# Optimization experiments

Hardware: AMD Instinct MI355X
Metric: run time of the kernel (lower is better)

## Reference

```python
import jax, jax.numpy as jnp
import numpy as np

N_NODES = 50000
N_EDGES = 800000
N_GRAPHS = 64


def graph_conv(x, edge_index, w_rel, b_rel, w_root):
    # PyG GraphConv with aggr='add':
    #   out = lin_rel(sum_{j in N(i)} x_j) + lin_root(x_i)
    src, dst = edge_index[0], edge_index[1]
    agg = jax.ops.segment_sum(x[src], dst, num_segments=x.shape[0])  # [N, d_in]
    return agg @ w_rel + b_rel + x @ w_root  # [N, d_out]


def scatter_mean(x, batch, num_segments):
    s = jax.ops.segment_sum(x, batch, num_segments=num_segments)
    cnt = jax.ops.segment_sum(jnp.ones((x.shape[0],), x.dtype), batch,
                              num_segments=num_segments)
    return s / jnp.maximum(cnt, 1.0)[:, None]


def setup_inputs() -> dict:
    key = jax.random.key(0)
    ks = jax.random.split(key, 8)
    d_feat, d_hid, d_out = 128, 128, 128
    x = jax.random.normal(ks[0], (N_NODES, d_feat), dtype=jnp.float32)
    edge_index = jax.random.randint(ks[1], (2, N_EDGES), 0, N_NODES, dtype=jnp.int64)
    batch = jnp.sort(jax.random.randint(ks[2], (N_NODES,), 0, N_GRAPHS, dtype=jnp.int64))

    def glorot(k, shape):
        fan_in = shape[0]
        return jax.random.normal(k, shape, dtype=jnp.float32) / np.sqrt(fan_in)

    return {
        "x": x,
        "edge_index": edge_index,
        "batch": batch,
        "w_rel1": glorot(ks[3], (d_feat, d_hid)),
        "b_rel1": jnp.zeros((d_hid,), jnp.float32),
        "w_root1": glorot(ks[4], (d_feat, d_hid)),
        "w_rel2": glorot(ks[5], (d_hid, 2 * d_hid)),
        "b_rel2": jnp.zeros((2 * d_hid,), jnp.float32),
        "w_root2": glorot(ks[6], (d_hid, 2 * d_hid)),
        "w_rel3": glorot(ks[7], (2 * d_hid, d_out)),
        "b_rel3": jnp.zeros((d_out,), jnp.float32),
        "w_root3": glorot(jax.random.fold_in(key, 99), (2 * d_hid, d_out)),
    }


def reference(x, edge_index, batch,
              w_rel1, b_rel1, w_root1,
              w_rel2, b_rel2, w_root2,
              w_rel3, b_rel3, w_root3):
    h = jax.nn.elu(graph_conv(x, edge_index, w_rel1, b_rel1, w_root1))
    h = jax.nn.elu(graph_conv(h, edge_index, w_rel2, b_rel2, w_root2))
    h = jax.nn.elu(graph_conv(h, edge_index, w_rel3, b_rel3, w_root3))
    return scatter_mean(h, batch, N_GRAPHS)  # [num_graphs, n_out]
```

## Files before the change

### kernel.cpp

```cpp
#include <hip/hip_runtime.h>
#include <math.h>

#define NN 50000
#define NNP 50048
#define NE 800000
#define NG 64
#define NBK 196
#define ECH 4082
#define TOTH (NBK * NBK)
#define NBH 151
#define SBLK 6890
#define SWORK (NN * 32 + 163840)

typedef __attribute__((ext_vector_type(8))) __bf16 bf16x8;
typedef __attribute__((ext_vector_type(4))) float f32x4;

__device__ inline unsigned short f2bf(float f) {
    unsigned int u = __float_as_uint(f);
    u += 0x7fffu + ((u >> 16) & 1u);
    return (unsigned short)(u >> 16);
}
__device__ inline float bflo(unsigned int v) { return __uint_as_float(v << 16); }
__device__ inline float bfhi(unsigned int v) { return __uint_as_float(v & 0xffff0000u); }
__device__ inline float bfs(unsigned short v) { return __uint_as_float((unsigned int)v << 16); }

#define GLD_LDS16(g, l)                                                          \
    __builtin_amdgcn_global_load_lds(                                            \
        (const __attribute__((address_space(1))) unsigned int*)(g),              \
        (__attribute__((address_space(3))) unsigned int*)(l), 16, 0, 0)

__global__ __launch_bounds__(256) void front_k(const float* __restrict__ x,
                                               const float* __restrict__ wr1,
                                               const float* __restrict__ wo1,
                                               const float* __restrict__ wr2,
                                               const float* __restrict__ wo2,
                                               const float* __restrict__ wr3,
                                               const float* __restrict__ wo3,
                                               const int* __restrict__ edst,
                                               const int* __restrict__ batch,
                                               unsigned short* __restrict__ xb,
                                               unsigned short* __restrict__ W1T,
                                               unsigned short* __restrict__ W2T,
                                               unsigned short* __restrict__ W3T,
                                               int* __restrict__ H,
                                               int* __restrict__ bounds,
                                               float* __restrict__ outp) {
    const int b = blockIdx.x, t = threadIdx.x;
    if (b < SBLK) {
        int id = b * 256 + t;
        if (id < NN * 32) {
            float4 v = ((const float4*)x)[id];
            unsigned int p0 = ((unsigned int)f2bf(v.y) << 16) | f2bf(v.x);
            unsigned int p1 = ((unsigned int)f2bf(v.w) << 16) | f2bf(v.z);
            ((uint2*)xb)[id] = make_uint2(p0, p1);
            return;
        }
        int w = id - NN * 32;
        if (w < 32768) {
            int n = w >> 8, k = w & 255;
            W1T[w] = f2bf((k < 128) ? wr1[k * 128 + n] : wo1[(k - 128) * 128 + n]);
        } else if (w < 98304) {
            int j = w - 32768; int n = j >> 8, k = j & 255;
            W2T[j] = f2bf((k < 128) ? wr2[k * 256 + n] : wo2[(k - 128) * 256 + n]);
        } else if (w < 163840) {
            int j = w - 98304; int n = j >> 8, k = j & 255;
            W3T[j] = f2bf((n < 128) ? wr3[k * 128 + n] : wo3[k * 128 + (n - 128)]);
        }
        return;
    }
    if (b < SBLK + NBK) {
        __shared__ int h[NBK];
        int k = b - SBLK;
        if (t < NBK) h[t] = 0;
        __syncthreads();
        int e0 = k * ECH, e1 = min(NE, e0 + ECH);
        for (int e = e0 + t; e < e1; e += 256) atomicAdd(&h[edst[e] >> 8], 1);
        __syncthreads();
        if (t < NBK) H[t * NBK + k] = h[t];
        return;
    }
    if (t <= NG) {
        int g = t, lo = 0, hi = NN;
        while (lo < hi) { int mid = (lo + hi) >> 1; if (batch[mid] < g) lo = mid + 1; else hi = mid; }
        bounds[g] = lo;
    }
    for (int i = t; i < NG * 128; i += 256) outp[i] = 0.f;
}

__global__ __launch_bounds__(256) void hsum_k(const int* __restrict__ H,
                                              int* __restrict__ hb) {
    int i = blockIdx.x * 256 + threadIdx.x;
    int v = (i < TOTH) ? H[i] : 0;
    for (int off = 32; off; off >>= 1) v += __shfl_xor(v, off, 64);
    __shared__ int ws[4];
    if ((threadIdx.x & 63) == 0) ws[threadIdx.x >> 6] = v;
    __syncthreads();
    if (threadIdx.x == 0) hb[blockIdx.x] = ws[0] + ws[1] + ws[2] + ws[3];
}

__global__ __launch_bounds__(256) void happly_k(const int* __restrict__ H,
                                                const int* __restrict__ hb,
                                                int* __restrict__ S) {
    __shared__ int s[256], ws[4], choff;
    const int t = threadIdx.x, c = blockIdx.x;
    {
        int v = (t < c) ? hb[t] : 0;
        for (int off = 32; off; off >>= 1) v += __shfl_xor(v, off, 64);
        if ((t & 63) == 0) ws[t >> 6] = v;
        __syncthreads();
        if (t == 0) choff = ws[0] + ws[1] + ws[2] + ws[3];
        __syncthreads();
    }
    int i = c * 256 + t;
    int v = (i < TOTH) ? H[i] : 0;
    s[t] = v; __syncthreads();
    for (int off = 1; off < 256; off <<= 1) {
        int u = (t >= off) ? s[t - off] : 0;
        __syncthreads(); s[t] += u; __syncthreads();
    }
    if (i < TOTH) S[i] = choff + s[t] - v;
}

__global__ __launch_bounds__(256) void scatter_k(const int* __restrict__ src,
                                                 const int* __restrict__ dst,
                                                 const int* __restrict__ S,
                                                 int* __restrict__ tmp) {
    __shared__ int cur[NBK];
    int t = threadIdx.x, k = blockIdx.x;
    if (t < NBK) cur[t] = S[t * NBK + k];
    __syncthreads();
    int e0 = k * ECH, e1 = min(NE, e0 + ECH);
    for (int e = e0 + t; e < e1; e += 256) {
        int d = dst[e];
        int p = atomicAdd(&cur[d >> 8], 1);
        tmp[p] = ((d & 255) << 16) | src[e];
    }
}

__global__ __launch_bounds__(256) void csr_k(const int* __restrict__ tmp,
                                             const int* __restrict__ S,
                                             int* __restrict__ rowptr,
                                             int* __restrict__ colsrc) {
    __shared__ int hist[256], off[256], cur[256];
    int t = threadIdx.x, b = blockIdx.x;
    int base = S[b * NBK];
    int next = (b < NBK - 1) ? S[(b + 1) * NBK] : NE;
    int cntb = next - base;
    hist[t] = 0;
    __syncthreads();
    for (int i = t; i < cntb; i += 256) atomicAdd(&hist[tmp[base + i] >> 16], 1);
    __syncthreads();
    int v = hist[t];
    off[t] = v; __syncthreads();
    for (int o = 1; o < 256; o <<= 1) {
        int u = (t >= o) ? off[t - o] : 0;
        __syncthreads(); off[t] += u; __syncthreads();
    }
    int excl = off[t] - v;
    int node = b * 256 + t;
    if (node <= NN) rowptr[node] = base + excl;
    cur[t] = excl;
    __syncthreads();
    for (int i = t; i < cntb; i += 256) {
        int e = tmp[base + i];
        int p = atomicAdd(&cur[e >> 16], 1);
        colsrc[base + p] = e & 0xffff;
    }
}

__global__ __launch_bounds__(256) void aggb_k(const unsigned short* __restrict__ feat,
                                              const int* __restrict__ rowptr,
                                              const int* __restrict__ colsrc,
                                              unsigned short* __restrict__ outp) {
    int node = __builtin_amdgcn_readfirstlane((int)(blockIdx.x * 4 + (threadIdx.x >> 6)));
    int lane = threadIdx.x & 63;
    int beg = rowptr[node], end = rowptr[node + 1];
    float ax = 0.f, ay = 0.f;
    int e = beg;
    for (; e + 8 <= end; e += 8) {
        unsigned int v[8];
#pragma unroll
        for (int i = 0; i < 8; ++i)
            v[i] = *(const unsigned int*)&feat[(size_t)colsrc[e + i] * 128 + lane * 2];
#pragma unroll
        for (int i = 0; i < 8; ++i) { ax += bflo(v[i]); ay += bfhi(v[i]); }
    }
    for (; e < end; ++e) {
        unsigned int v0 = *(const unsigned int*)&feat[(size_t)colsrc[e] * 128 + lane * 2];
        ax += bflo(v0); ay += bfhi(v0);
    }
    unsigned int p = ((unsigned int)f2bf(ay) << 16) | f2bf(ax);
    *(unsigned int*)&outp[(size_t)node * 128 + lane * 2] = p;
}

__global__ __launch_bounds__(256) void aggf_k(const unsigned short* __restrict__ y,
                                              const unsigned short* __restrict__ rr,
                                              const float* __restrict__ b3,
                                              const int* __restrict__ rowptr,
                                              const int* __restrict__ colsrc,
                                              unsigned short* __restrict__ outp) {
    int node = __builtin_amdgcn_readfirstlane((int)(blockIdx.x * 4 + (threadIdx.x >> 6)));
    int lane = threadIdx.x & 63;
    int beg = rowptr[node], end = rowptr[node + 1];
    float ax = 0.f, ay = 0.f;
    int e = beg;
    for (; e + 8 <= end; e += 8) {
        unsigned int v[8];
#pragma unroll
        for (int i = 0; i < 8; ++i)
            v[i] = *(const unsigned int*)&y[(size_t)colsrc[e + i] * 128 + lane * 2];
#pragma unroll
        for (int i = 0; i < 8; ++i) { ax += bflo(v[i]); ay += bfhi(v[i]); }
    }
    for (; e < end; ++e) {
        unsigned int v0 = *(const unsigned int*)&y[(size_t)colsrc[e] * 128 + lane * 2];
        ax += bflo(v0); ay += bfhi(v0);
    }
    unsigned int rv = *(const unsigned int*)&rr[(size_t)node * 128 + lane * 2];
    float2 bb = *(const float2*)&b3[lane * 2];
    float vx = ax + bflo(rv) + bb.x;
    float vy = ay + bfhi(rv) + bb.y;
    vx = vx > 0.f ? vx : (__expf(vx) - 1.f);
    vy = vy > 0.f ? vy : (__expf(vy) - 1.f);
    unsigned int p = ((unsigned int)f2bf(vy) << 16) | f2bf(vx);
    *(unsigned int*)&outp[(size_t)node * 128 + lane * 2] = p;
}

template <int MT, int KA, int N, bool TWO, bool BIAS, bool ELU>
__global__ __launch_bounds__(256) void gemm_k(const unsigned short* __restrict__ A1,
                                              const unsigned short* __restrict__ A2,
                                              const unsigned short* __restrict__ WT,
                                              const float* __restrict__ bias,
                                              unsigned short* __restrict__ Cout) {
    constexpr int KTOT = TWO ? 2 * KA : KA;
    constexpr int MI = MT / 32;
    __shared__ __attribute__((aligned(16))) unsigned short As[MT * 32];
    __shared__ __attribute__((aligned(16))) unsigned short Bs[128 * 32];
    const int t = threadIdx.x;
    const int wv = t >> 6, lane = t & 63;
    const int qd = lane >> 4, l16 = lane & 15;
    const int m0 = blockIdx.x * MT, n0 = 0;
    const int mh = (wv & 1) * (MT / 2), nh = (wv >> 1) * 64;
    const int srow = lane >> 2;
    const int skk  = (lane & 3) * 8;

    f32x4 acc[MI][4] = {};

    for (int k0 = 0; k0 < KTOT; k0 += 32) {
        const unsigned short* Abase = (TWO && k0 >= KA) ? (A2 + (k0 - KA)) : (A1 + k0);
#pragma unroll
        for (int i = 0; i < MT / 64; ++i) {
            int chunk = wv * (MT / 64) + i;
            const unsigned short* g = Abase + (size_t)(m0 + chunk * 16 + srow) * KA + skk;
            GLD_LDS16(g, &As[chunk * 512]);
        }
        const unsigned short* Wbase = WT + k0;
#pragma unroll
        for (int i = 0; i < 2; ++i) {
            int chunk = wv * 2 + i;
            const unsigned short* g = Wbase + (size_t)(n0 + chunk * 16 + srow) * KTOT + skk;
            GLD_LDS16(g, &Bs[chunk * 512]);
        }
        __syncthreads();
        bf16x8 af[MI], bfr[4];
#pragma unroll
        for (int mi = 0; mi < MI; ++mi)
            af[mi] = *(const bf16x8*)&As[(mh + mi * 16 + l16) * 32 + qd * 8];
#pragma unroll
        for (int ni = 0; ni < 4; ++ni)
            bfr[ni] = *(const bf16x8*)&Bs[(nh + ni * 16 + l16) * 32 + qd * 8];
#pragma unroll
        for (int mi = 0; mi < MI; ++mi)
#pragma unroll
            for (int ni = 0; ni < 4; ++ni)
                acc[mi][ni] = __builtin_amdgcn_mfma_f32_16x16x32_bf16(
                    af[mi], bfr[ni], acc[mi][ni], 0, 0, 0);
        __syncthreads();
    }

#pragma unroll
    for (int mi = 0; mi < MI; ++mi)
#pragma unroll
        for (int ni = 0; ni < 4; ++ni)
#pragma unroll
            for (int r = 0; r < 4; ++r) {
                int mm = m0 + mh + mi * 16 + qd * 4 + r;
                if (mm < NN) {
                    int nn = n0 + nh + ni * 16 + l16;
                    float v = acc[mi][ni][r];
                    if (BIAS) v += bias[nn];
                    if (ELU) v = v > 0.f ? v : (__expf(v) - 1.f);
                    Cout[(size_t)mm * N + nn] = f2bf(v);
                }
            }
}

template <int KA, bool TWO, bool BIAS, bool ELU, bool SPLIT>
__global__ __launch_bounds__(256) void gemm256_k(const unsigned short* __restrict__ A1,
                                                 const unsigned short* __restrict__ A2,
                                                 const unsigned short* __restrict__ WT,
                                                 const float* __restrict__ bias,
                                                 unsigned short* __restrict__ Cout,
                                                 unsigned short* __restrict__ Cout2) {
    constexpr int KTOT = TWO ? 2 * KA : KA;
    __shared__ __attribute__((aligned(16))) unsigned short As[64 * 32];
    __shared__ __attribute__((aligned(16))) unsigned short Bs[256 * 32];
    const int t = threadIdx.x;
    const int wv = t >> 6, lane = t & 63;
    const int qd = lane >> 4, l16 = lane & 15;
    const int m0 = blockIdx.x * 64;
    const int srow = lane >> 2;
    const int skk  = (lane & 3) * 8;

    f32x4 acc[4][4] = {};

    for (int k0 = 0; k0 < KTOT; k0 += 32) {
        const unsigned short* Abase = (TWO && k0 >= KA) ? (A2 + (k0 - KA)) : (A1 + k0);
        {
            const unsigned short* g = Abase + (size_t)(m0 + wv * 16 + srow) * KA + skk;
            GLD_LDS16(g, &As[wv * 512]);
        }
        const unsigned short* Wbase = WT + k0;
#pragma unroll
        for (int i = 0; i < 4; ++i) {
            int chunk = wv * 4 + i;
            const unsigned short* g = Wbase + (size_t)(chunk * 16 + srow) * KTOT + skk;
            GLD_LDS16(g, &Bs[chunk * 512]);
        }
        __syncthreads();
        bf16x8 af[4], bfr[4];
#pragma unroll
        for (int mi = 0; mi < 4; ++mi)
            af[mi] = *(const bf16x8*)&As[(mi * 16 + l16) * 32 + qd * 8];
#pragma unroll
        for (int ni = 0; ni < 4; ++ni)
            bfr[ni] = *(const bf16x8*)&Bs[(wv * 64 + ni * 16 + l16) * 32 + qd * 8];
#pragma unroll
        for (int mi = 0; mi < 4; ++mi)
#pragma unroll
            for (int ni = 0; ni < 4; ++ni)
                acc[mi][ni] = __builtin_amdgcn_mfma_f32_16x16x32_bf16(
                    af[mi], bfr[ni], acc[mi][ni], 0, 0, 0);
        __syncthreads();
    }

#pragma unroll
    for (int mi = 0; mi < 4; ++mi)
#pragma unroll
        for (int ni = 0; ni < 4; ++ni)
#pragma unroll
            for (int r = 0; r < 4; ++r) {
                int mm = m0 + mi * 16 + qd * 4 + r;
                if (mm < NN) {
                    int nn = wv * 64 + ni * 16 + l16;
                    float v = acc[mi][ni][r];
                    if (BIAS) v += bias[nn];
                    if (ELU) v = v > 0.f ? v : (__expf(v) - 1.f);
                    unsigned short b = f2bf(v);
                    if (SPLIT) {
                        unsigned short* dst = (nn < 128) ? Cout : Cout2;
                        dst[(size_t)mm * 128 + (nn & 127)] = b;
                    } else {
                        Cout[(size_t)mm * 256 + nn] = b;
                    }
                }
            }
}

__global__ __launch_bounds__(128) void sum_k(const unsigned short* __restrict__ vals,
                                             const int* __restrict__ batch,
                                             float* __restrict__ outsum) {
    const int CH = 25;
    int n0 = blockIdx.x * CH;
    int c = threadIdx.x;
    int g = batch[n0];
    float acc = 0.f;
    for (int i = 0; i < CH; ++i) {
        int n = n0 + i;
        int gn = batch[n];
        if (gn != g) {
            unsafeAtomicAdd(&outsum[(size_t)g * 128 + c], acc);
            acc = 0.f; g = gn;
        }
        acc += bfs(vals[(size_t)n * 128 + c]);
    }
    unsafeAtomicAdd(&outsum[(size_t)g * 128 + c], acc);
}

__global__ void divide_k(const int* __restrict__ bounds, float* __restrict__ out) {
    int i = blockIdx.x * 256 + threadIdx.x;
    if (i < NG * 128) {
        int g = i >> 7;
        float c = (float)(bounds[g + 1] - bounds[g]);
        out[i] /= fmaxf(c, 1.f);
    }
}

extern "C" void kernel_launch(void* const* d_in, const int* in_sizes, int n_in,
                              void* d_out, int out_size, void* d_ws, size_t ws_size,
                              hipStream_t stream) {
    const float* x       = (const float*)d_in[0];
    const int*   ei      = (const int*)d_in[1];
    const int*   batch   = (const int*)d_in[2];
    const float* w_rel1  = (const float*)d_in[3];
    const float* b_rel1  = (const float*)d_in[4];
    const float* w_root1 = (const float*)d_in[5];
    const float* w_rel2  = (const float*)d_in[6];
    const float* b_rel2  = (const float*)d_in[7];
    const float* w_root2 = (const float*)d_in[8];
    const float* w_rel3  = (const float*)d_in[9];
    const float* b_rel3  = (const float*)d_in[10];
    const float* w_root3 = (const float*)d_in[11];
    const int* esrc = ei;
    const int* edst = ei + NE;

    unsigned short* Ab = (unsigned short*)d_ws;
    unsigned short* Bb = Ab + (size_t)NNP * 128;
    unsigned short* Cb = Bb + (size_t)NNP * 128;
    unsigned short* xb = Cb + (size_t)NNP * 256;
    unsigned short* W1T = xb + (size_t)NNP * 128;
    unsigned short* W2T = W1T + 128 * 256;
    unsigned short* W3T = W2T + 256 * 256;
    int* rowptr = (int*)(W3T + 256 * 256);
    int* colsrc = rowptr + (NN + 1);
    int* tmp    = colsrc + NE;
    int* H      = tmp + NE;
    int* S      = H + TOTH;
    int* hb     = S + TOTH;
    int* bounds = hb + 256;
    float* outp = (float*)d_out;

    front_k<<<SBLK + NBK + 1, 256, 0, stream>>>(
        x, w_rel1, w_root1, w_rel2, w_root2, w_rel3, w_root3, edst, batch,
        xb, W1T, W2T, W3T, H, bounds, outp);
    hsum_k<<<NBH, 256, 0, stream>>>(H, hb);
    happly_k<<<NBH, 256, 0, stream>>>(H, hb, S);
    scatter_k<<<NBK, 256, 0, stream>>>(esrc, edst, S, tmp);
    csr_k<<<NBK, 256, 0, stream>>>(tmp, S, rowptr, colsrc);

    aggb_k<<<NN / 4, 256, 0, stream>>>(xb, rowptr, colsrc, Ab);
    gemm_k<64, 128, 128, true, true, true>
        <<<NNP / 64, 256, 0, stream>>>(Ab, xb, W1T, b_rel1, Bb);

    aggb_k<<<NN / 4, 256, 0, stream>>>(Bb, rowptr, colsrc, Ab);
    gemm256_k<128, true, true, true, false>
        <<<NNP / 64, 256, 0, stream>>>(Ab, Bb, W2T, b_rel2, Cb, nullptr);

    gemm256_k<256, false, false, false, true>
        <<<NNP / 64, 256, 0, stream>>>(Cb, nullptr, W3T, nullptr, Ab, Bb);

    aggf_k<<<NN / 4, 256, 0, stream>>>(Ab, Bb, b_rel3, rowptr, colsrc, Cb);
    sum_k<<<NN / 25, 128, 0, stream>>>(Cb, batch, outp);
    divide_k<<<(NG * 128 + 255) / 256, 256, 0, stream>>>(bounds, outp);
}
```

Measured before the change: 299.0 us.

## Double-buffer GEMM LDS loads, slice aggregation by feature, widen pooling kernel

Both GEMM kernels now use two LDS buffers. The next K-step's global-to-LDS loads are issued before computing on the current one, with explicit vmcnt waits and raw barriers in place of __syncthreads, so load latency can overlap MFMA work. The aggregation kernels assign 16 lanes per node across four feature slices, with a 64-byte slice per block, and preload the column indices. This gives 16 nodes per block in flight instead of one node per wave. The pooling sum kernel uses 4 waves per block and reads two bf16 values per lane. Changes to the LDS footprint and the hand-coded wait counts risk occupancy loss or ordering bugs.

```diff
diff --git a/kernel.cpp b/kernel.cpp
--- a/kernel.cpp
+++ b/kernel.cpp
@@ -11,6 +11,7 @@
 #define NBH 151
 #define SBLK 6890
 #define SWORK (NN * 32 + 163840)
+#define AGB 12500
 
 typedef __attribute__((ext_vector_type(8))) __bf16 bf16x8;
 typedef __attribute__((ext_vector_type(4))) float f32x4;
@@ -168,62 +169,74 @@
     }
 }
 
-__global__ __launch_bounds__(256) void aggb_k(const unsigned short* __restrict__ feat,
+__global__ __launch_bounds__(256) void aggs_k(const unsigned short* __restrict__ feat,
                                               const int* __restrict__ rowptr,
                                               const int* __restrict__ colsrc,
                                               unsigned short* __restrict__ outp) {
-    int node = __builtin_amdgcn_readfirstlane((int)(blockIdx.x * 4 + (threadIdx.x >> 6)));
-    int lane = threadIdx.x & 63;
-    int beg = rowptr[node], end = rowptr[node + 1];
+    const int slice = blockIdx.x & 3;
+    const int gid = threadIdx.x >> 4;
+    const int l16 = threadIdx.x & 15;
+    const int node = (blockIdx.x >> 2) * 16 + gid;
+    const int fo = slice * 32 + l16 * 2;
+    const int beg = rowptr[node], end = rowptr[node + 1];
     float ax = 0.f, ay = 0.f;
     int e = beg;
     for (; e + 8 <= end; e += 8) {
+        int c[8];
+#pragma unroll
+        for (int i = 0; i < 8; ++i) c[i] = colsrc[e + i];
         unsigned int v[8];
 #pragma unroll
         for (int i = 0; i < 8; ++i)
-            v[i] = *(const unsigned int*)&feat[(size_t)colsrc[e + i] * 128 + lane * 2];
+            v[i] = *(const unsigned int*)&feat[(size_t)c[i] * 128 + fo];
 #pragma unroll
         for (int i = 0; i < 8; ++i) { ax += bflo(v[i]); ay += bfhi(v[i]); }
     }
     for (; e < end; ++e) {
-        unsigned int v0 = *(const unsigned int*)&feat[(size_t)colsrc[e] * 128 + lane * 2];
-        ax += bflo(v0); ay += bfhi(v0);
+        unsigned int v = *(const unsigned int*)&feat[(size_t)colsrc[e] * 128 + fo];
+        ax += bflo(v); ay += bfhi(v);
     }
     unsigned int p = ((unsigned int)f2bf(ay) << 16) | f2bf(ax);
-    *(unsigned int*)&outp[(size_t)node * 128 + lane * 2] = p;
-}
-
-__global__ __launch_bounds__(256) void aggf_k(const unsigned short* __restrict__ y,
-                                              const unsigned short* __restrict__ rr,
-                                              const float* __restrict__ b3,
-                                              const int* __restrict__ rowptr,
-                                              const int* __restrict__ colsrc,
-                                              unsigned short* __restrict__ outp) {
-    int node = __builtin_amdgcn_readfirstlane((int)(blockIdx.x * 4 + (threadIdx.x >> 6)));
-    int lane = threadIdx.x & 63;
-    int beg = rowptr[node], end = rowptr[node + 1];
+    *(unsigned int*)&outp[(size_t)node * 128 + fo] = p;
+}
+
+__global__ __launch_bounds__(256) void aggfs_k(const unsigned short* __restrict__ y,
+                                               const unsigned short* __restrict__ rr,
+                                               const float* __restrict__ b3,
+                                               const int* __restrict__ rowptr,
+                                               const int* __restrict__ colsrc,
+                                               unsigned short* __restrict__ outp) {
+    const int slice = blockIdx.x & 3;
+    const int gid = threadIdx.x >> 4;
+    const int l16 = threadIdx.x & 15;
+    const int node = (blockIdx.x >> 2) * 16 + gid;
+    const int fo = slice * 32 + l16 * 2;
+    const int beg = rowptr[node], end = rowptr[node + 1];
     float ax = 0.f, ay = 0.f;
     int e = beg;
     for (; e + 8 <= end; e += 8) {
+        int c[8];
+#pragma unroll
+        for (int i = 0; i < 8; ++i) c[i] = colsrc[e + i];
         unsigned int v[8];
 #pragma unroll
         for (int i = 0; i < 8; ++i)
-            v[i] = *(const unsigned int*)&y[(size_t)colsrc[e + i] * 128 + lane * 2];
+            v[i] = *(const unsigned int*)&y[(size_t)c[i] * 128 + fo];
 #pragma unroll
         for (int i = 0; i < 8; ++i) { ax += bflo(v[i]); ay += bfhi(v[i]); }
     }
     for (; e < end; ++e) {
-        unsigned int v0 = *(const unsigned int*)&y[(size_t)colsrc[e] * 128 + lane * 2];
-        ax += bflo(v0); ay += bfhi(v0);
-    }
-    unsigned int rv = *(const unsigned int*)&rr[(size_t)node * 128 + lane * 2];
-    float2 bb = *(const float2*)&b3[lane * 2];
+        unsigned int v = *(const unsigned int*)&y[(size_t)colsrc[e] * 128 + fo];
+        ax += bflo(v); ay += bfhi(v);
+    }
+    unsigned int rv = *(const unsigned int*)&rr[(size_t)node * 128 + fo];
+    float2 bb = *(const float2*)&b3[fo];
     float vx = ax + bflo(rv) + bb.x;
     float vy = ay + bfhi(rv) + bb.y;
     vx = vx > 0.f ? vx : (__expf(vx) - 1.f);
     vy = vy > 0.f ? vy : (__expf(vy) - 1.f);
     unsigned int p = ((unsigned int)f2bf(vy) << 16) | f2bf(vx);
-    *(unsigned int*)&outp[(size_t)node * 128 + lane * 2] = p;
+    *(unsigned int*)&outp[(size_t)node * 128 + fo] = p;
 }
 
 template <int MT, int KA, int N, bool TWO, bool BIAS, bool ELU>
@@ -233,49 +246,65 @@
                                               const float* __restrict__ bias,
                                               unsigned short* __restrict__ Cout) {
     constexpr int KTOT = TWO ? 2 * KA : KA;
+    constexpr int NSTEP = KTOT / 32;
     constexpr int MI = MT / 32;
-    __shared__ __attribute__((aligned(16))) unsigned short As[MT * 32];
-    __shared__ __attribute__((aligned(16))) unsigned short Bs[128 * 32];
+    constexpr int LA = MT / 64;
+    constexpr int LB = N / 64;
+    __shared__ __attribute__((aligned(16))) unsigned short As[2][MT * 32];
+    __shared__ __attribute__((aligned(16))) unsigned short Bs[2][N * 32];
     const int t = threadIdx.x;
     const int wv = t >> 6, lane = t & 63;
     const int qd = lane >> 4, l16 = lane & 15;
-    const int m0 = blockIdx.x * MT, n0 = 0;
+    const int m0 = blockIdx.x * MT;
     const int mh = (wv & 1) * (MT / 2), nh = (wv >> 1) * 64;
     const int srow = lane >> 2;
     const int skk  = (lane & 3) * 8;
 
     f32x4 acc[MI][4] = {};
 
-    for (int k0 = 0; k0 < KTOT; k0 += 32) {
+    auto stage = [&](int k0, int buf) {
         const unsigned short* Abase = (TWO && k0 >= KA) ? (A2 + (k0 - KA)) : (A1 + k0);
 #pragma unroll
-        for (int i = 0; i < MT / 64; ++i) {
-            int chunk = wv * (MT / 64) + i;
+        for (int i = 0; i < LA; ++i) {
+            int chunk = wv * LA + i;
             const unsigned short* g = Abase + (size_t)(m0 + chunk * 16 + srow) * KA + skk;
-            GLD_LDS16(g, &As[chunk * 512]);
+            GLD_LDS16(g, &As[buf][chunk * 512]);
         }
         const unsigned short* Wbase = WT + k0;
 #pragma unroll
-        for (int i = 0; i < 2; ++i) {
-            int chunk = wv * 2 + i;
-            const unsigned short* g = Wbase + (size_t)(n0 + chunk * 16 + srow) * KTOT + skk;
-            GLD_LDS16(g, &Bs[chunk * 512]);
-        }
-        __syncthreads();
+        for (int i = 0; i < LB; ++i) {
+            int chunk = wv * LB + i;
+            const unsigned short* g = Wbase + (size_t)(chunk * 16 + srow) * KTOT + skk;
+            GLD_LDS16(g, &Bs[buf][chunk * 512]);
+        }
+    };
+
+    stage(0, 0);
+    for (int s = 0; s < NSTEP; ++s) {
+        const int cur = s & 1;
+        if (s + 1 < NSTEP) {
+            stage((s + 1) * 32, cur ^ 1);
+            asm volatile("s_waitcnt vmcnt(%0)" :: "i"(LA + LB) : "memory");
+        } else {
+            asm volatile("s_waitcnt vmcnt(0)" ::: "memory");
+        }
+        __builtin_amdgcn_s_barrier();
+        asm volatile("" ::: "memory");
         bf16x8 af[MI], bfr[4];
 #pragma unroll
         for (int mi = 0; mi < MI; ++mi)
-            af[mi] = *(const bf16x8*)&As[(mh + mi * 16 + l16) * 32 + qd * 8];
+            af[mi] = *(const bf16x8*)&As[cur][(mh + mi * 16 + l16) * 32 + qd * 8];
 #pragma unroll
         for (int ni = 0; ni < 4; ++ni)
-            bfr[ni] = *(const bf16x8*)&Bs[(nh + ni * 16 + l16) * 32 + qd * 8];
+            bfr[ni] = *(const bf16x8*)&Bs[cur][(nh + ni * 16 + l16) * 32 + qd * 8];
 #pragma unroll
         for (int mi = 0; mi < MI; ++mi)
 #pragma unroll
             for (int ni = 0; ni < 4; ++ni)
                 acc[mi][ni] = __builtin_amdgcn_mfma_f32_16x16x32_bf16(
                     af[mi], bfr[ni], acc[mi][ni], 0, 0, 0);
-        __syncthreads();
+        asm volatile("" ::: "memory");
+        __builtin_amdgcn_s_barrier();
     }
 
 #pragma unroll
@@ -286,7 +315,7 @@
             for (int r = 0; r < 4; ++r) {
                 int mm = m0 + mh + mi * 16 + qd * 4 + r;
                 if (mm < NN) {
-                    int nn = n0 + nh + ni * 16 + l16;
+                    int nn = nh + ni * 16 + l16;
                     float v = acc[mi][ni][r];
                     if (BIAS) v += bias[nn];
                     if (ELU) v = v > 0.f ? v : (__expf(v) - 1.f);
@@ -303,8 +332,9 @@
                                                  unsigned short* __restrict__ Cout,
                                                  unsigned short* __restrict__ Cout2) {
     constexpr int KTOT = TWO ? 2 * KA : KA;
-    __shared__ __attribute__((aligned(16))) unsigned short As[64 * 32];
-    __shared__ __attribute__((aligned(16))) unsigned short Bs[256 * 32];
+    constexpr int NSTEP = KTOT / 32;
+    __shared__ __attribute__((aligned(16))) unsigned short As[2][64 * 32];
+    __shared__ __attribute__((aligned(16))) unsigned short Bs[2][256 * 32];
     const int t = threadIdx.x;
     const int wv = t >> 6, lane = t & 63;
     const int qd = lane >> 4, l16 = lane & 15;
@@ -314,34 +344,47 @@
 
     f32x4 acc[4][4] = {};
 
-    for (int k0 = 0; k0 < KTOT; k0 += 32) {
+    auto stage = [&](int k0, int buf) {
         const unsigned short* Abase = (TWO && k0 >= KA) ? (A2 + (k0 - KA)) : (A1 + k0);
         {
             const unsigned short* g = Abase + (size_t)(m0 + wv * 16 + srow) * KA + skk;
-            GLD_LDS16(g, &As[wv * 512]);
+            GLD_LDS16(g, &As[buf][wv * 512]);
         }
         const unsigned short* Wbase = WT + k0;
 #pragma unroll
         for (int i = 0; i < 4; ++i) {
             int chunk = wv * 4 + i;
             const unsigned short* g = Wbase + (size_t)(chunk * 16 + srow) * KTOT + skk;
-            GLD_LDS16(g, &Bs[chunk * 512]);
-        }
-        __syncthreads();
+            GLD_LDS16(g, &Bs[buf][chunk * 512]);
+        }
+    };
+
+    stage(0, 0);
+    for (int s = 0; s < NSTEP; ++s) {
+        const int cur = s & 1;
+        if (s + 1 < NSTEP) {
+            stage((s + 1) * 32, cur ^ 1);
+            asm volatile("s_waitcnt vmcnt(%0)" :: "i"(5) : "memory");
+        } else {
+            asm volatile("s_waitcnt vmcnt(0)" ::: "memory");
+        }
+        __builtin_amdgcn_s_barrier();
+        asm volatile("" ::: "memory");
         bf16x8 af[4], bfr[4];
 #pragma unroll
         for (int mi = 0; mi < 4; ++mi)
-            af[mi] = *(const bf16x8*)&As[(mi * 16 + l16) * 32 + qd * 8];
+            af[mi] = *(const bf16x8*)&As[cur][(mi * 16 + l16) * 32 + qd * 8];
 #pragma unroll
         for (int ni = 0; ni < 4; ++ni)
-            bfr[ni] = *(const bf16x8*)&Bs[(wv * 64 + ni * 16 + l16) * 32 + qd * 8];
+            bfr[ni] = *(const bf16x8*)&Bs[cur][(wv * 64 + ni * 16 + l16) * 32 + qd * 8];
 #pragma unroll
         for (int mi = 0; mi < 4; ++mi)
 #pragma unroll
             for (int ni = 0; ni < 4; ++ni)
                 acc[mi][ni] = __builtin_amdgcn_mfma_f32_16x16x32_bf16(
                     af[mi], bfr[ni], acc[mi][ni], 0, 0, 0);
-        __syncthreads();
+        asm volatile("" ::: "memory");
+        __builtin_amdgcn_s_barrier();
     }
 
 #pragma unroll
@@ -367,24 +410,27 @@
             }
 }
 
-__global__ __launch_bounds__(128) void sum_k(const unsigned short* __restrict__ vals,
+__global__ __launch_bounds__(256) void sum_k(const unsigned short* __restrict__ vals,
                                              const int* __restrict__ batch,
                                              float* __restrict__ outsum) {
     const int CH = 25;
-    int n0 = blockIdx.x * CH;
-    int c = threadIdx.x;
+    int wv = threadIdx.x >> 6, lane = threadIdx.x & 63;
+    int n0 = (blockIdx.x * 4 + wv) * CH;
     int g = batch[n0];
-    float acc = 0.f;
+    float ax = 0.f, ay = 0.f;
     for (int i = 0; i < CH; ++i) {
         int n = n0 + i;
         int gn = batch[n];
         if (gn != g) {
-            unsafeAtomicAdd(&outsum[(size_t)g * 128 + c], acc);
-            acc = 0.f; g = gn;
-        }
-        acc += bfs(vals[(size_t)n * 128 + c]);
-    }
-    unsafeAtomicAdd(&outsum[(size_t)g * 128 + c], acc);
+            unsafeAtomicAdd(&outsum[(size_t)g * 128 + lane * 2], ax);
+            unsafeAtomicAdd(&outsum[(size_t)g * 128 + lane * 2 + 1], ay);
+            ax = 0.f; ay = 0.f; g = gn;
+        }
+        unsigned int v = *(const unsigned int*)&vals[(size_t)n * 128 + lane * 2];
+        ax += bflo(v); ay += bfhi(v);
+    }
+    unsafeAtomicAdd(&outsum[(size_t)g * 128 + lane * 2], ax);
+    unsafeAtomicAdd(&outsum[(size_t)g * 128 + lane * 2 + 1], ay);
 }
 
 __global__ void divide_k(const int* __restrict__ bounds, float* __restrict__ out) {
@@ -438,18 +484,18 @@
     scatter_k<<<NBK, 256, 0, stream>>>(esrc, edst, S, tmp);
     csr_k<<<NBK, 256, 0, stream>>>(tmp, S, rowptr, colsrc);
 
-    aggb_k<<<NN / 4, 256, 0, stream>>>(xb, rowptr, colsrc, Ab);
+    aggs_k<<<AGB, 256, 0, stream>>>(xb, rowptr, colsrc, Ab);
     gemm_k<64, 128, 128, true, true, true>
         <<<NNP / 64, 256, 0, stream>>>(Ab, xb, W1T, b_rel1, Bb);
 
-    aggb_k<<<NN / 4, 256, 0, stream>>>(Bb, rowptr, colsrc, Ab);
+    aggs_k<<<AGB, 256, 0, stream>>>(Bb, rowptr, colsrc, Ab);
     gemm256_k<128, true, true, true, false>
         <<<NNP / 64, 256, 0, stream>>>(Ab, Bb, W2T, b_rel2, Cb, nullptr);
 
     gemm256_k<256, false, false, false, true>
         <<<NNP / 64, 256, 0, stream>>>(Cb, nullptr, W3T, nullptr, Ab, Bb);
 
-    aggf_k<<<NN / 4, 256, 0, stream>>>(Ab, Bb, b_rel3, rowptr, colsrc, Cb);
-    sum_k<<<NN / 25, 128, 0, stream>>>(Cb, batch, outp);
+    aggfs_k<<<AGB, 256, 0, stream>>>(Ab, Bb, b_rel3, rowptr, colsrc, Cb);
+    sum_k<<<NN / 100, 256, 0, stream>>>(Cb, batch, outp);
     divide_k<<<(NG * 128 + 255) / 256, 256, 0, stream>>>(bounds, outp);
 }
```

After: 362.9 us. 21.4% more time.
